# Optimization experiments

Measured on AMD Instinct MI355X. Metric: run time of the kernel, lower is better.

## Reference

```python
import jax, jax.numpy as jnp
import numpy as np

DN = ('NCHW', 'OIHW', 'NCHW')
LAP = jnp.array([[0., -1., 0.], [-1., 4., -1.], [0., -1., 0.]], dtype=jnp.float32).reshape(1, 1, 3, 3)
CH, NE = 24, 256


def conv(x, w, stride=1, pad=0):
    return jax.lax.conv_general_dilated(x, w, (stride, stride), ((pad, pad), (pad, pad)), dimension_numbers=DN)


def conv_t(x, w):
    # torch ConvTranspose2d(k=4, s=2, p=1); w is torch layout [in, out, 4, 4]
    wt = jnp.flip(w, (2, 3)).transpose(1, 0, 2, 3)
    return jax.lax.conv_general_dilated(x, wt, (1, 1), ((2, 2), (2, 2)), lhs_dilation=(2, 2), dimension_numbers=DN)


def spatial_attn(x, w_sa):
    y = jnp.concatenate([jnp.mean(x, 1, keepdims=True), jnp.max(x, 1, keepdims=True)], 1)
    return x * jax.nn.sigmoid(conv(y, w_sa, pad=3))


def res_branch(x, wr, wp, wsa):
    k = wr.shape[-1]
    h = conv(x, wr, pad=k // 2)
    h = conv(h, wp)
    return jax.nn.relu(spatial_attn(h, wsa))


def enc_block(x, wr, wp, wsa, wout):
    x = x + res_branch(x, wr, wp, wsa)
    return conv(x, wout, stride=2, pad=1)


def dec_block(x, wr, wp, wsa, wout):
    x = conv_t(x, wout)
    return x + res_branch(x, wr, wp, wsa)


def quantize(inp, embed):
    # inp: [B,H,W,D] tokens, embed: [D,N] codebook
    f = inp.reshape(-1, inp.shape[-1])
    dist = (f * f).sum(1, keepdims=True) - 2.0 * (f @ embed) + (embed * embed).sum(0, keepdims=True)
    ind = jnp.argmin(dist, axis=1)
    q = jnp.take(embed.T, ind, axis=0).reshape(inp.shape)
    diff = jnp.mean((jax.lax.stop_gradient(q) - inp) ** 2)
    q = inp + jax.lax.stop_gradient(q - inp)  # straight-through
    return q, diff


def _forward(x, w_img_in, w_img_out,
             w_res_et, w_pw_et, w_sa_et, w_out_et,
             w_res_em, w_pw_em, w_sa_em, w_out_em,
             w_res_ed, w_pw_ed, w_sa_ed, w_out_ed,
             w_res_dt, w_pw_dt, w_sa_dt, w_out_dt,
             w_res_dm, w_pw_dm, w_sa_dm, w_out_dm,
             w_res_dd, w_pw_dd, w_sa_dd, w_out_dd,
             w_squ1, w_squ2, embed2, embed3):
    xl = jax.lax.stop_gradient(conv(jnp.mean(x, 1, keepdims=True), LAP, pad=1))
    h = conv(xl, w_img_in)
    enc1 = enc_block(h, w_res_et, w_pw_et, w_sa_et, w_out_et)      # H/2
    enc2 = enc_block(enc1, w_res_em, w_pw_em, w_sa_em, w_out_em)   # H/4
    enc3 = enc_block(enc2, w_res_ed, w_pw_ed, w_sa_ed, w_out_ed)   # H/8
    qt2, d2 = quantize(enc2.transpose(0, 2, 3, 1), embed2)
    qt2 = qt2.transpose(0, 3, 1, 2)
    qt3, d3 = quantize(enc3.transpose(0, 2, 3, 1), embed3)
    qt3 = qt3.transpose(0, 3, 1, 2)
    dec3 = dec_block(qt3, w_res_dd, w_pw_dd, w_sa_dd, w_out_dd)    # H/4
    dec2 = conv(jnp.concatenate([dec3, qt2], 1), w_squ2)
    dec2 = dec_block(dec2, w_res_dm, w_pw_dm, w_sa_dm, w_out_dm)   # H/2
    dec1 = conv(jnp.concatenate([dec2, enc1], 1), w_squ1)
    dec1 = dec_block(dec1, w_res_dt, w_pw_dt, w_sa_dt, w_out_dt)   # H
    mask_lap = conv(dec1, w_img_out)
    clean_lap = xl - mask_lap
    return mask_lap, clean_lap, (d2 + d3).reshape(1)


def _param_shapes():
    shapes = {'w_img_in': (CH, 1, 1, 1), 'w_img_out': (1, CH, 1, 1),
              'w_squ1': (CH, 2 * CH, 1, 1), 'w_squ2': (CH, 2 * CH, 1, 1),
              'embed2': (CH, NE), 'embed3': (CH, NE)}
    for tag, k in [('et', 7), ('em', 5), ('ed', 3), ('dt', 7), ('dm', 5), ('dd', 3)]:
        shapes['w_res_' + tag] = (CH, CH, k, k)
        shapes['w_pw_' + tag] = (CH, CH, 1, 1)
        shapes['w_sa_' + tag] = (1, 2, 7, 7)
        shapes['w_out_' + tag] = (CH, CH, 4, 4)
    return shapes


def setup_inputs() -> dict:
    key = jax.random.key(0)
    shapes = _param_shapes()
    names = sorted(shapes)
    keys = jax.random.split(key, len(names) + 1)
    inputs = {'x': jax.random.normal(keys[0], (8, 3, 512, 512), dtype=jnp.float32)}
    for k_, name in zip(keys[1:], names):
        w = jax.random.normal(k_, shapes[name], dtype=jnp.float32)
        if not name.startswith('embed'):
            w = w * 0.05  # conv weight init scale
        inputs[name] = w
    return inputs


def reference(x, embed2, embed3, w_img_in, w_img_out,
              w_out_dd, w_out_dm, w_out_dt, w_out_ed, w_out_em, w_out_et,
              w_pw_dd, w_pw_dm, w_pw_dt, w_pw_ed, w_pw_em, w_pw_et,
              w_res_dd, w_res_dm, w_res_dt, w_res_ed, w_res_em, w_res_et,
              w_sa_dd, w_sa_dm, w_sa_dt, w_sa_ed, w_sa_em, w_sa_et,
              w_squ1, w_squ2):
    return _forward(x, w_img_in, w_img_out,
                    w_res_et, w_pw_et, w_sa_et, w_out_et,
                    w_res_em, w_pw_em, w_sa_em, w_out_em,
                    w_res_ed, w_pw_ed, w_sa_ed, w_out_ed,
                    w_res_dt, w_pw_dt, w_sa_dt, w_out_dt,
                    w_res_dm, w_pw_dm, w_sa_dm, w_out_dm,
                    w_res_dd, w_pw_dd, w_sa_dd, w_out_dd,
                    w_squ1, w_squ2, embed2, embed3)
```

## Files before the change

### kernel.cpp

```cpp
#include <hip/hip_runtime.h>
#include <math.h>

#define CH 24

typedef __attribute__((ext_vector_type(8))) short short8v;
typedef __attribute__((ext_vector_type(4))) float f32x4;
typedef unsigned short ushort_t;
typedef unsigned int uint_t;

__device__ inline ushort_t bf16r(float f){
  uint_t u = __float_as_uint(f);
  u += 0x7FFF + ((u>>16)&1);
  return (ushort_t)(u>>16);
}
__device__ inline float bf2f(uint_t u){ return __uint_as_float(u<<16); }

__global__ void k_r_res(const float* __restrict__ w, float* __restrict__ wT, int K){
  int i = blockIdx.x*256 + threadIdx.x;
  int n = 576*K*K; if (i >= n) return;
  int co = i % 24, ci = (i/24) % 24, kk = i/576;
  int ky = kk / K, kx = kk % K;
  wT[i] = w[((co*24+ci)*K+ky)*K+kx];
}
__global__ void k_r_pw(const float* __restrict__ w, float* __restrict__ wT, int CIN){
  int i = blockIdx.x*256 + threadIdx.x;
  if (i >= CIN*24) return;
  int co = i % 24, ci = i/24;
  wT[i] = w[co*CIN+ci];
}
__global__ void k_rmfma(const float* __restrict__ w, ushort_t* __restrict__ wb, int K){
  int i = blockIdx.x*256 + threadIdx.x;
  int n = K*K*1024; if (i >= n) return;
  int j = i & 7, l = (i>>3) & 63, t = (i>>9) & 1, tap = i >> 10;
  int ci = (l>>4)*8 + j, co = t*16 + (l&15);
  int ky = tap / K, kx = tap % K;
  float v = (ci<24 && co<24) ? w[((co*24+ci)*K+ky)*K+kx] : 0.f;
  wb[i] = bf16r(v);
}
__global__ void k_rmfma4(const float* __restrict__ w, ushort_t* __restrict__ wb){
  int i = blockIdx.x*256 + threadIdx.x;
  if (i >= 16384) return;
  int j = i & 7, l = (i>>3) & 63, t = (i>>9) & 1, tap = i >> 10;
  int ci = (l>>4)*8 + j, co = t*16 + (l&15);
  int ky = tap >> 2, kx = tap & 3;
  float v = (ci<24 && co<24) ? w[((ci*24+co)*4+ky)*4+kx] : 0.f;
  wb[i] = bf16r(v);
}


__global__ void k_lap(const float* __restrict__ x, float* __restrict__ xl, int H, int W){
  int idx = blockIdx.x*256 + threadIdx.x;
  int HW = H*W;
  if (idx >= HW) return;
  const float* xb = x + (size_t)blockIdx.z*3*HW;
  float* xo = xl + (size_t)blockIdx.z*HW;
  int px = idx % W, py = idx / W;
#define MEANV(yy,xx) (((yy)>=0&&(yy)<H&&(xx)>=0&&(xx)<W) ? (xb[(yy)*W+(xx)]+xb[HW+(yy)*W+(xx)]+xb[2*HW+(yy)*W+(xx)])*(1.f/3.f) : 0.f)
  float v = 4.f*MEANV(py,px) - MEANV(py-1,px) - MEANV(py+1,px) - MEANV(py,px-1) - MEANV(py,px+1);
#undef MEANV
  xo[idx] = v;
}

template<int K, bool EXPAND, bool INBF, bool OUTBF>
__launch_bounds__(512)
__global__ void k_conv_mfma(const void* in, const ushort_t* __restrict__ wb,
                            const ushort_t* __restrict__ wbpw, const float* __restrict__ wexp,
                            void* out, float* __restrict__ mm,
                            int H, int W, int istrIn, int istrOut, int istrMM){
  constexpr int SW_T = 32 + K - 1;
  constexpr int SH = 16 + K - 1;
  constexpr int NPX = SH*SW_T;
  __shared__ ushort_t lds[NPX*24];
  __shared__ uint_t sc[8][16*20];
  int tid = threadIdx.x;
  const float* inb_f = (const float*)in + (size_t)blockIdx.z*istrIn;
  const ushort_t* inb_b = (const ushort_t*)in + (size_t)blockIdx.z*istrIn;
  int x0g = blockIdx.x*32 - K/2, y0g = blockIdx.y*16 - K/2;
  int HW = H*W;
  for (int i = tid; i < NPX*3; i += 512){
    int q = i / NPX;
    int pp = i - q*NPX;
    int row = pp / SW_T, col = pp - row*SW_T;
    int gy = y0g + row, gx = x0g + col;
    uint4 w4; w4.x=0u; w4.y=0u; w4.z=0u; w4.w=0u;
    if (gy >= 0 && gy < H && gx >= 0 && gx < W){
      size_t base = (size_t)gy*W + gx;
      int c0 = q*8;
      if (EXPAND){
        float val = inb_f[base];
        w4.x = (uint_t)bf16r(val*wexp[c0+0]) | ((uint_t)bf16r(val*wexp[c0+1])<<16);
        w4.y = (uint_t)bf16r(val*wexp[c0+2]) | ((uint_t)bf16r(val*wexp[c0+3])<<16);
        w4.z = (uint_t)bf16r(val*wexp[c0+4]) | ((uint_t)bf16r(val*wexp[c0+5])<<16);
        w4.w = (uint_t)bf16r(val*wexp[c0+6]) | ((uint_t)bf16r(val*wexp[c0+7])<<16);
      } else if (INBF){
        uint_t u0=inb_b[(size_t)(c0+0)*HW+base], u1=inb_b[(size_t)(c0+1)*HW+base];
        uint_t u2=inb_b[(size_t)(c0+2)*HW+base], u3=inb_b[(size_t)(c0+3)*HW+base];
        uint_t u4=inb_b[(size_t)(c0+4)*HW+base], u5=inb_b[(size_t)(c0+5)*HW+base];
        uint_t u6=inb_b[(size_t)(c0+6)*HW+base], u7=inb_b[(size_t)(c0+7)*HW+base];
        w4.x = u0 | (u1<<16); w4.y = u2 | (u3<<16); w4.z = u4 | (u5<<16); w4.w = u6 | (u7<<16);
      } else {
        w4.x = (uint_t)bf16r(inb_f[(size_t)(c0+0)*HW+base]) | ((uint_t)bf16r(inb_f[(size_t)(c0+1)*HW+base])<<16);
        w4.y = (uint_t)bf16r(inb_f[(size_t)(c0+2)*HW+base]) | ((uint_t)bf16r(inb_f[(size_t)(c0+3)*HW+base])<<16);
        w4.z = (uint_t)bf16r(inb_f[(size_t)(c0+4)*HW+base]) | ((uint_t)bf16r(inb_f[(size_t)(c0+5)*HW+base])<<16);
        w4.w = (uint_t)bf16r(inb_f[(size_t)(c0+6)*HW+base]) | ((uint_t)bf16r(inb_f[(size_t)(c0+7)*HW+base])<<16);
      }
    }
// ... 192 lines not shown
}

template<bool INBF, bool OUTBF>
__launch_bounds__(512)
__global__ void k_down_mfma(const void* in, const ushort_t* __restrict__ wb,
                            void* out, int Ho, int Wo, int istrIn, int istrOut){
  const int Hi = Ho*2, Wi = Wo*2;
  constexpr int NPX = 18*34;
  __shared__ ushort_t lds[NPX*24];
  int tid = threadIdx.x;
  const float* inb_f = (const float*)in + (size_t)blockIdx.z*istrIn;
  const ushort_t* inb_b = (const ushort_t*)in + (size_t)blockIdx.z*istrIn;
  int X0 = blockIdx.x*16, Y0 = blockIdx.y*8;
  int ix0 = 2*X0 - 1, iy0 = 2*Y0 - 1;
  int HWi = Hi*Wi;
  for (int i = tid; i < NPX*3; i += 512){
    int q = i / NPX;
    int pp = i - q*NPX;
    int row = pp / 34;
    int rem = pp - row*34;
    int par = (rem >= 17) ? 1 : 0;
    int sub = rem - par*17;
    int gx = ix0 + 2*sub + par;
    int gy = iy0 + row;
    uint4 w4; w4.x=0u; w4.y=0u; w4.z=0u; w4.w=0u;
    if (gy>=0 && gy<Hi && gx>=0 && gx<Wi){
      size_t base = (size_t)gy*Wi + gx;
      int c0 = q*8;
      if (INBF){
        uint_t u0=inb_b[(size_t)(c0+0)*HWi+base], u1=inb_b[(size_t)(c0+1)*HWi+base];
        uint_t u2=inb_b[(size_t)(c0+2)*HWi+base], u3=inb_b[(size_t)(c0+3)*HWi+base];
        uint_t u4=inb_b[(size_t)(c0+4)*HWi+base], u5=inb_b[(size_t)(c0+5)*HWi+base];
        uint_t u6=inb_b[(size_t)(c0+6)*HWi+base], u7=inb_b[(size_t)(c0+7)*HWi+base];
        w4.x = u0 | (u1<<16); w4.y = u2 | (u3<<16); w4.z = u4 | (u5<<16); w4.w = u6 | (u7<<16);
      } else {
        w4.x = (uint_t)bf16r(inb_f[(size_t)(c0+0)*HWi+base]) | ((uint_t)bf16r(inb_f[(size_t)(c0+1)*HWi+base])<<16);
        w4.y = (uint_t)bf16r(inb_f[(size_t)(c0+2)*HWi+base]) | ((uint_t)bf16r(inb_f[(size_t)(c0+3)*HWi+base])<<16);
        w4.z = (uint_t)bf16r(inb_f[(size_t)(c0+4)*HWi+base]) | ((uint_t)bf16r(inb_f[(size_t)(c0+5)*HWi+base])<<16);
        w4.w = (uint_t)bf16r(inb_f[(size_t)(c0+6)*HWi+base]) | ((uint_t)bf16r(inb_f[(size_t)(c0+7)*HWi+base])<<16);
      }
    }
    *(uint4*)(lds + (size_t)pp*24 + q*8) = w4;
  }
  __syncthreads();
  int l = tid & 63, wid = tid >> 6;
  int kg = l >> 4, li = l & 15;
  int kgc = (kg < 3) ? kg : 2;
  f32x4 zero = {0.f,0.f,0.f,0.f};
  f32x4 acc0 = zero, acc1 = zero;
  const ushort_t* aln = lds + li*24 + kgc*8 + (size_t)(2*wid)*34*24;
  #pragma unroll
  for (int ky=0; ky<4; ky++){
    #pragma unroll
    for (int kx=0; kx<4; kx++){
      int tap = ky*4 + kx;
      const ushort_t* wp = wb + (size_t)tap*1024;
      short8v b0 = *(const short8v*)(wp + l*8);
      short8v b1 = *(const short8v*)(wp + 512 + l*8);
      short8v a = *(const short8v*)(aln + (ky*34 + (kx&1)*17 + (kx>>1))*24);
      acc0 = __builtin_amdgcn_mfma_f32_16x16x32_bf16(a, b0, acc0, 0, 0, 0);
      acc1 = __builtin_amdgcn_mfma_f32_16x16x32_bf16(a, b1, acc1, 0, 0, 0);
    }
  }
  int HWo = Ho*Wo;
  int oy = Y0 + wid, ox = X0 + kg*4;
  if (OUTBF){
    ushort_t* outb = (ushort_t*)out + (size_t)blockIdx.z*istrOut;
    uint2 p0; p0.x = (uint_t)bf16r(acc0[0]) | ((uint_t)bf16r(acc0[1])<<16);
    p0.y = (uint_t)bf16r(acc0[2]) | ((uint_t)bf16r(acc0[3])<<16);
    *(uint2*)(outb + (size_t)li*HWo + (size_t)oy*Wo + ox) = p0;
    if (li < 8){
      uint2 p1; p1.x = (uint_t)bf16r(acc1[0]) | ((uint_t)bf16r(acc1[1])<<16);
      p1.y = (uint_t)bf16r(acc1[2]) | ((uint_t)bf16r(acc1[3])<<16);
      *(uint2*)(outb + (size_t)(16+li)*HWo + (size_t)oy*Wo + ox) = p1;
    }
  } else {
    float* outb = (float*)out + (size_t)blockIdx.z*istrOut;
    *(f32x4*)(outb + (size_t)li*HWo + (size_t)oy*Wo + ox) = acc0;
    if (li < 8)
      *(f32x4*)(outb + (size_t)(16+li)*HWo + (size_t)oy*Wo + ox) = acc1;
  }
}

template<int K, int TH>
__launch_bounds__(256)
__global__ void k_conv(const float* __restrict__ in, const float* __restrict__ wT,
                       float* __restrict__ out, int H, int W, int istrIn, int istrOut){
  constexpr int TW = 32;
  constexpr int PX = (TW*TH)/256;
  constexpr int XT = TW/PX;
  constexpr int SW = TW + K - 1;
  constexpr int SWP = SW | 1;
  constexpr int SH = TH + K - 1;
  constexpr int CC = 8;
  __shared__ float tile[CC*SH*SWP];
  int tx = threadIdx.x % XT, ty = threadIdx.x / XT;
  int x0 = blockIdx.x*TW - K/2, y0 = blockIdx.y*TH - K/2;
  const float* inb = in + (size_t)blockIdx.z*istrIn;
  float acc[CH][PX];
  #pragma unroll
  for (int co=0;co<CH;co++)
    #pragma unroll
    for (int px=0;px<PX;px++) acc[co][px] = 0.f;

  #pragma unroll 1
  for (int c0=0;c0<CH;c0+=CC){
    __syncthreads();
    for (int i=threadIdx.x; i<CC*SH*SW; i+=256){
      int col = i % SW; int rr = i / SW; int row = rr % SH; int c = rr / SH;
      int gy = y0+row, gx = x0+col;
      tile[(c*SH+row)*SWP+col] = (gy>=0 && gy<H && gx>=0 && gx<W)
          ? inb[(size_t)(c0+c)*H*W + (size_t)gy*W + gx] : 0.f;
    }
    __syncthreads();
    #pragma unroll 1
    for (int ci=0;ci<CC;ci++){
      #pragma unroll 1
      for (int ky=0;ky<K;ky++){
        const float* trow = &tile[(ci*SH + ty+ky)*SWP + tx*PX];
        #pragma unroll
        for (int kx=0;kx<K;kx++){
          float v[PX];
          #pragma unroll
          for (int px=0;px<PX;px++) v[px] = trow[kx+px];
          const float* wp = wT + ((ky*K+kx)*24 + c0+ci)*24;
          #pragma unroll
          for (int co=0;co<CH;co++){
            float wv = wp[co];
            #pragma unroll
            for (int px=0;px<PX;px++) acc[co][px] = fmaf(v[px], wv, acc[co][px]);
          }
        }
      }
    }
  }
  int oy = blockIdx.y*TH+ty, ox = blockIdx.x*TW+tx*PX;
  float* ob = out + (size_t)blockIdx.z*istrOut + (size_t)oy*W + ox;
  #pragma unroll
  for (int co=0;co<CH;co++){
    if (PX == 2){
      float2 o; o.x=acc[co][0]; o.y=acc[co][1];
      *(float2*)(ob + (size_t)co*H*W) = o;
    } else {
      ob[(size_t)co*H*W] = acc[co][0];
    }
  }
}

__global__ void k_pw(const float* in, const float* __restrict__ wT,
                     float* out, float* __restrict__ mm, int HW, int istr, int istrMM){
  int p = (blockIdx.x*256 + threadIdx.x)*4;
  if (p >= HW) return;
  const float* ib = in + (size_t)blockIdx.z*istr;
  float acc[CH][4];
  #pragma unroll
  for (int co=0;co<CH;co++){ acc[co][0]=0;acc[co][1]=0;acc[co][2]=0;acc[co][3]=0; }
  #pragma unroll 1
  for (int ci=0;ci<CH;ci++){
    float4 v = *(const float4*)(ib + (size_t)ci*HW + p);
    const float* wp = wT + ci*24;
    #pragma unroll
    for (int co=0;co<CH;co++){
      float wv = wp[co];
      acc[co][0] = fmaf(v.x, wv, acc[co][0]);
      acc[co][1] = fmaf(v.y, wv, acc[co][1]);
      acc[co][2] = fmaf(v.z, wv, acc[co][2]);
      acc[co][3] = fmaf(v.w, wv, acc[co][3]);
    }
  }
  float mean[4]={0,0,0,0}, mx[4]={-3.4e38f,-3.4e38f,-3.4e38f,-3.4e38f};
  #pragma unroll
  for (int co=0;co<CH;co++)
    #pragma unroll
    for (int j=0;j<4;j++){ mean[j]+=acc[co][j]; mx[j]=fmaxf(mx[j],acc[co][j]); }
  float* ob = out + (size_t)blockIdx.z*istr;
  #pragma unroll
  for (int co=0;co<CH;co++){
    float4 o; o.x=acc[co][0]; o.y=acc[co][1]; o.z=acc[co][2]; o.w=acc[co][3];
    *(float4*)(ob + (size_t)co*HW + p) = o;
  }
  float* mb = mm + (size_t)blockIdx.z*istrMM;
  float4 me; me.x=mean[0]*(1.f/24.f); me.y=mean[1]*(1.f/24.f); me.z=mean[2]*(1.f/24.f); me.w=mean[3]*(1.f/24.f);
  float4 mxo; mxo.x=mx[0]; mxo.y=mx[1]; mxo.z=mx[2]; mxo.w=mx[3];
  *(float4*)(mb + p) = me;
  *(float4*)(mb + HW + p) = mxo;
}

template<bool BF>
__global__ void k_attn_res(const void* R_, const float* __restrict__ M,
                           const void* X_, const float* __restrict__ wsa,
                           void* out_, int H, int W, int istr, int istrMM){
  int p = (blockIdx.x*256 + threadIdx.x)*4;
  int HW = H*W;
  if (p >= HW) return;
  int py = p / W, px0 = p % W;
  const float* Mb = M + (size_t)blockIdx.z*istrMM;
  float s[4]={0,0,0,0};
  #pragma unroll
  for (int cc=0;cc<2;cc++){
    const float* Mc = Mb + (size_t)cc*HW;
    #pragma unroll 1
    for (int ky=0;ky<7;ky++){
      int gy = py+ky-3;
      if (gy<0||gy>=H) continue;
      const float* mr = Mc + (size_t)gy*W;
      float mv[10];
      #pragma unroll
      for (int j=0;j<10;j++){
        int gx = px0-3+j;
        mv[j] = (gx>=0 && gx<W) ? mr[gx] : 0.f;
      }
      const float* wr = wsa + (cc*7+ky)*7;
      #pragma unroll
      for (int kx=0;kx<7;kx++){
        float wv = wr[kx];
        #pragma unroll
        for (int px=0;px<4;px++) s[px] = fmaf(mv[kx+px], wv, s[px]);
      }
    }
  }
  float g[4];
  #pragma unroll
  for (int px=0;px<4;px++) g[px] = 1.f/(1.f+expf(-s[px]));
  #pragma unroll
  for (int c=0;c<CH;c++){
    float r0,r1,r2,r3, x0v,x1v,x2v,x3v;
    if (BF){
      const ushort_t* Rb = (const ushort_t*)R_ + (size_t)blockIdx.z*istr + (size_t)c*HW + p;
      const ushort_t* Xb = (const ushort_t*)X_ + (size_t)blockIdx.z*istr + (size_t)c*HW + p;
      uint2 rv = *(const uint2*)Rb;
      uint2 xv = *(const uint2*)Xb;
      r0=bf2f(rv.x&0xffffu); r1=bf2f(rv.x>>16); r2=bf2f(rv.y&0xffffu); r3=bf2f(rv.y>>16);
      x0v=bf2f(xv.x&0xffffu); x1v=bf2f(xv.x>>16); x2v=bf2f(xv.y&0xffffu); x3v=bf2f(xv.y>>16);
    } else {
      const float* Rb = (const float*)R_ + (size_t)blockIdx.z*istr + (size_t)c*HW + p;
      const float* Xb = (const float*)X_ + (size_t)blockIdx.z*istr + (size_t)c*HW + p;
      float4 rv = *(const float4*)Rb;
      float4 xv = *(const float4*)Xb;
      r0=rv.x; r1=rv.y; r2=rv.z; r3=rv.w;
      x0v=xv.x; x1v=xv.y; x2v=xv.z; x3v=xv.w;
    }
    float o0 = x0v + fmaxf(r0*g[0], 0.f);
    float o1 = x1v + fmaxf(r1*g[1], 0.f);
    float o2 = x2v + fmaxf(r2*g[2], 0.f);
    float o3 = x3v + fmaxf(r3*g[3], 0.f);
    if (BF){
      ushort_t* Ob = (ushort_t*)out_ + (size_t)blockIdx.z*istr + (size_t)c*HW + p;
      uint2 ov;
      ov.x = (uint_t)bf16r(o0) | ((uint_t)bf16r(o1)<<16);
      ov.y = (uint_t)bf16r(o2) | ((uint_t)bf16r(o3)<<16);
      *(uint2*)Ob = ov;
    } else {
      float* Ob = (float*)out_ + (size_t)blockIdx.z*istr + (size_t)c*HW + p;
      float4 ov; ov.x=o0; ov.y=o1; ov.z=o2; ov.w=o3;
      *(float4*)Ob = ov;
    }
  }
}

template<bool BF>
__global__ void k_attn_res_x(const void* R_, const float* __restrict__ M,
                             const float* __restrict__ XL, const float* __restrict__ wsa,
                             const float* __restrict__ wexp,
                             void* out_, int H, int W, int istr, int istrMM){
  int p = (blockIdx.x*256 + threadIdx.x)*4;
  int HW = H*W;
  if (p >= HW) return;
  int py = p / W, px0 = p % W;
  const float* Mb = M + (size_t)blockIdx.z*istrMM;
  float s[4]={0,0,0,0};
  #pragma unroll
  for (int cc=0;cc<2;cc++){
    const float* Mc = Mb + (size_t)cc*HW;
    #pragma unroll 1
    for (int ky=0;ky<7;ky++){
      int gy = py+ky-3;
      if (gy<0||gy>=H) continue;
      const float* mr = Mc + (size_t)gy*W;
      float mv[10];
      #pragma unroll
      for (int j=0;j<10;j++){
        int gx = px0-3+j;
        mv[j] = (gx>=0 && gx<W) ? mr[gx] : 0.f;
      }
      const float* wr = wsa + (cc*7+ky)*7;
      #pragma unroll
      for (int kx=0;kx<7;kx++){
        float wv = wr[kx];
        #pragma unroll
        for (int px=0;px<4;px++) s[px] = fmaf(mv[kx+px], wv, s[px]);
      }
    }
  }
  float g[4];
  #pragma unroll
  for (int px=0;px<4;px++) g[px] = 1.f/(1.f+expf(-s[px]));
  float4 xl4 = *(const float4*)(XL + (size_t)blockIdx.z*HW + p);
  #pragma unroll
  for (int c=0;c<CH;c++){
    float wc = wexp[c];
    float r0,r1,r2,r3;
    if (BF){
      const ushort_t* Rb = (const ushort_t*)R_ + (size_t)blockIdx.z*istr + (size_t)c*HW + p;
      uint2 rv = *(const uint2*)Rb;
      r0=bf2f(rv.x&0xffffu); r1=bf2f(rv.x>>16); r2=bf2f(rv.y&0xffffu); r3=bf2f(rv.y>>16);
    } else {
      const float* Rb = (const float*)R_ + (size_t)blockIdx.z*istr + (size_t)c*HW + p;
      float4 rv = *(const float4*)Rb;
      r0=rv.x; r1=rv.y; r2=rv.z; r3=rv.w;
    }
    float o0 = xl4.x*wc + fmaxf(r0*g[0], 0.f);
    float o1 = xl4.y*wc + fmaxf(r1*g[1], 0.f);
    float o2 = xl4.z*wc + fmaxf(r2*g[2], 0.f);
    float o3 = xl4.w*wc + fmaxf(r3*g[3], 0.f);
    if (BF){
      ushort_t* Ob = (ushort_t*)out_ + (size_t)blockIdx.z*istr + (size_t)c*HW + p;
      uint2 ov;
      ov.x = (uint_t)bf16r(o0) | ((uint_t)bf16r(o1)<<16);
      ov.y = (uint_t)bf16r(o2) | ((uint_t)bf16r(o3)<<16);
      *(uint2*)Ob = ov;
    } else {
      float* Ob = (float*)out_ + (size_t)blockIdx.z*istr + (size_t)c*HW + p;
      float4 ov; ov.x=o0; ov.y=o1; ov.z=o2; ov.w=o3;
      *(float4*)Ob = ov;
    }
  }
}

template<bool BF>
__global__ void k_squeeze(const void* inA_, const void* inB_,
                          const float* __restrict__ wT, void* out_, int HW, int istr){
  int p = (blockIdx.x*256 + threadIdx.x)*4;
  if (p >= HW) return;
  float acc[CH][4];
  #pragma unroll
  for (int co=0;co<CH;co++){ acc[co][0]=0;acc[co][1]=0;acc[co][2]=0;acc[co][3]=0; }
  #pragma unroll 1
  for (int ci=0;ci<48;ci++){
    float v0,v1,v2,v3;
    if (BF){
      const ushort_t* src = (ci<24)
        ? ((const ushort_t*)inA_ + (size_t)blockIdx.z*istr + (size_t)ci*HW + p)
        : ((const ushort_t*)inB_ + (size_t)blockIdx.z*istr + (size_t)(ci-24)*HW + p);
      uint2 rv = *(const uint2*)src;
      v0=bf2f(rv.x&0xffffu); v1=bf2f(rv.x>>16); v2=bf2f(rv.y&0xffffu); v3=bf2f(rv.y>>16);
    } else {
      const float* src = (ci<24)
        ? ((const float*)inA_ + (size_t)blockIdx.z*istr + (size_t)ci*HW + p)
        : ((const float*)inB_ + (size_t)blockIdx.z*istr + (size_t)(ci-24)*HW + p);
      float4 rv = *(const float4*)src;
      v0=rv.x; v1=rv.y; v2=rv.z; v3=rv.w;
    }
    const float* wp = wT + ci*24;
    #pragma unroll
    for (int co=0;co<CH;co++){
      float wv = wp[co];
      acc[co][0] = fmaf(v0, wv, acc[co][0]);
      acc[co][1] = fmaf(v1, wv, acc[co][1]);
      acc[co][2] = fmaf(v2, wv, acc[co][2]);
      acc[co][3] = fmaf(v3, wv, acc[co][3]);
    }
  }
  #pragma unroll
  for (int co=0;co<CH;co++){
    if (BF){
      ushort_t* ob = (ushort_t*)out_ + (size_t)blockIdx.z*istr + (size_t)co*HW + p;
      uint2 ov;
      ov.x = (uint_t)bf16r(acc[co][0]) | ((uint_t)bf16r(acc[co][1])<<16);
      ov.y = (uint_t)bf16r(acc[co][2]) | ((uint_t)bf16r(acc[co][3])<<16);
      *(uint2*)ob = ov;
    } else {
      float* ob = (float*)out_ + (size_t)blockIdx.z*istr + (size_t)co*HW + p;
      float4 o; o.x=acc[co][0]; o.y=acc[co][1]; o.z=acc[co][2]; o.w=acc[co][3];
      *(float4*)ob = o;
    }
  }
}

__global__ void k_quant(const float* __restrict__ enc, const float* __restrict__ embed,
                        float* __restrict__ qt, float* __restrict__ diffAcc, int HW, int istr){
  __shared__ float em[256*28];
  __shared__ float red[4];
  {
    int j = threadIdx.x;
    float s = 0.f;
    #pragma unroll
    for (int c=0;c<CH;c++){
      float e = embed[c*256+j];
      em[j*28+c] = -2.0f*e;
      s = fmaf(e,e,s);
    }
    em[j*28+24] = s; em[j*28+25]=0.f; em[j*28+26]=0.f; em[j*28+27]=0.f;
  }
  __syncthreads();
  int p = blockIdx.x*256 + threadIdx.x;
  const float* eb = enc + (size_t)blockIdx.z*istr;
  float f[CH];
  #pragma unroll
  for (int c=0;c<CH;c++) f[c] = eb[(size_t)c*HW + p];
  float best = 3.4e38f; int bj = 0;
  #pragma unroll 1
  for (int j=0;j<256;j++){
    const float4* row = (const float4*)&em[j*28];
    float s = em[j*28+24];
    #pragma unroll
    for (int q4=0;q4<6;q4++){
      float4 r = row[q4];
      s = fmaf(f[q4*4+0], r.x, s);
      s = fmaf(f[q4*4+1], r.y, s);
      s = fmaf(f[q4*4+2], r.z, s);
      s = fmaf(f[q4*4+3], r.w, s);
    }
    if (s < best){ best = s; bj = j; }
  }
  float* qb = qt + (size_t)blockIdx.z*istr;
  float d = 0.f;
  #pragma unroll
  for (int c=0;c<CH;c++){
    float q = embed[c*256+bj];
    qb[(size_t)c*HW + p] = q;
    float e = q - f[c];
    d = fmaf(e,e,d);
  }
  #pragma unroll
  for (int off=32; off>0; off>>=1) d += __shfl_down(d, off, 64);
  int lane = threadIdx.x & 63, wv = threadIdx.x >> 6;
  if (lane==0) red[wv] = d;
  __syncthreads();
  if (threadIdx.x==0) atomicAdd(diffAcc, red[0]+red[1]+red[2]+red[3]);
}

__global__ void k_final(const ushort_t* __restrict__ dec1, const float* __restrict__ w,
                        const float* __restrict__ xl, float* __restrict__ outMask,
                        float* __restrict__ outClean, int HW, int dstr){
  int p = (blockIdx.x*256 + threadIdx.x)*4;
  if (p >= HW) return;
  const ushort_t* db = dec1 + (size_t)blockIdx.z*dstr;
  float m[4]={0,0,0,0};
  #pragma unroll
  for (int c=0;c<CH;c++){
    uint2 dv = *(const uint2*)(db + (size_t)c*HW + p);
    float wc = w[c];
    m[0]=fmaf(bf2f(dv.x&0xffffu),wc,m[0]);
    m[1]=fmaf(bf2f(dv.x>>16),wc,m[1]);
    m[2]=fmaf(bf2f(dv.y&0xffffu),wc,m[2]);
    m[3]=fmaf(bf2f(dv.y>>16),wc,m[3]);
  }
  float4 xv = *(const float4*)(xl + (size_t)blockIdx.z*HW + p);
  float4 mo; mo.x=m[0]; mo.y=m[1]; mo.z=m[2]; mo.w=m[3];
  float4 co; co.x=xv.x-m[0]; co.y=xv.y-m[1]; co.z=xv.z-m[2]; co.w=xv.w-m[3];
  *(float4*)(outMask + (size_t)blockIdx.z*HW + p) = mo;
  *(float4*)(outClean + (size_t)blockIdx.z*HW + p) = co;
}

__global__ void k_diff(const float* __restrict__ acc, float* __restrict__ out){
  out[0] = acc[0]*(1.f/3145728.f) + acc[1]*(1.f/786432.f);
}

extern "C" void kernel_launch(void* const* d_in, const int* in_sizes, int n_in,
                              void* d_out, int out_size, void* d_ws, size_t ws_size,
                              hipStream_t stream) {
  const float* x        = (const float*)d_in[0];
  const float* embed2   = (const float*)d_in[1];
  const float* embed3   = (const float*)d_in[2];
  const float* w_img_in = (const float*)d_in[3];
  const float* w_img_out= (const float*)d_in[4];
  const float* w_out_dd = (const float*)d_in[5];
  const float* w_out_dm = (const float*)d_in[6];
  const float* w_out_dt = (const float*)d_in[7];
  const float* w_out_ed = (const float*)d_in[8];
  const float* w_out_em = (const float*)d_in[9];
  const float* w_out_et = (const float*)d_in[10];
  const float* w_pw_dd  = (const float*)d_in[11];
  const float* w_pw_dm  = (const float*)d_in[12];
  const float* w_pw_dt  = (const float*)d_in[13];
  const float* w_pw_ed  = (const float*)d_in[14];
  const float* w_pw_em  = (const float*)d_in[15];
  const float* w_pw_et  = (const float*)d_in[16];
  const float* w_res_dd = (const float*)d_in[17];
  const float* w_res_dm = (const float*)d_in[18];
  const float* w_res_dt = (const float*)d_in[19];
  const float* w_res_ed = (const float*)d_in[20];
  const float* w_res_em = (const float*)d_in[21];
  const float* w_res_et = (const float*)d_in[22];
  const float* w_sa_dd  = (const float*)d_in[23];
  const float* w_sa_dm  = (const float*)d_in[24];
  const float* w_sa_dt  = (const float*)d_in[25];
  const float* w_sa_ed  = (const float*)d_in[26];
  const float* w_sa_em  = (const float*)d_in[27];
  const float* w_sa_et  = (const float*)d_in[28];
  const float* w_squ1   = (const float*)d_in[29];
  const float* w_squ2   = (const float*)d_in[30];
  (void)in_sizes; (void)n_in; (void)out_size;

  const int HW512 = 512*512, HW256 = 256*256, HW128 = 128*128, HW64 = 64*64;
  const int S512 = 24*HW512, S256 = 24*HW256, S128 = 24*HW128, S64 = 24*HW64;

  float* ws = (float*)d_ws;
  float* OUT = (float*)d_out;
  size_t F = ws_size / sizeof(float);

  float* WT      = ws;
  float* wt_ed3  = WT + 85248;
  float* wt_dd3  = WT + 90432;
  float* wt_pw_ed= WT + 152064;
  float* wt_pw_dd= WT + 152640;
  float* wt_squ1 = WT + 154368;
  float* wt_squ2 = WT + 155520;

  ushort_t* WB = (ushort_t*)(ws + 160000);
  ushort_t* wb_et7   = WB;
  ushort_t* wb_dt7   = WB + 50176;
  ushort_t* wb_em5   = WB + 100352;
  ushort_t* wb_dm5   = WB + 125952;
  ushort_t* wb_pw_et = WB + 151552;
  ushort_t* wb_pw_em = WB + 152576;
  ushort_t* wb_pw_dm = WB + 153600;
  ushort_t* wb_pw_dt = WB + 154624;
  ushort_t* wb4_dd   = WB + 155648;
  ushort_t* wb4_dm   = WB + 172032;
  ushort_t* wb4_dt   = WB + 188416;
  ushort_t* wb4d_et  = WB + 204800;
  ushort_t* wb4d_em  = WB + 221184;
  ushort_t* wb4d_ed  = WB + 237568;

  const size_t ABASE = 290000;

  auto needBatched = [&](size_t CB)->size_t{
    size_t u_f = (CB*(size_t)S512 + 1)/2;
    if ((size_t)4*S256 > u_f) u_f = (size_t)4*S256;
    if ((size_t)8*S128 > u_f) u_f = (size_t)8*S128;
    return ABASE + 2097152 + (size_t)4*S256 + 3145728 + 786432 + CB*524288 + 2*u_f + 2;
  };
  int CB = 0;
  if (F >= needBatched(8)) CB = 8;
  else if (F >= needBatched(4)) CB = 4;
  else if (F >= needBatched(2)) CB = 2;
  const size_t NEED_B = ABASE + 15925250;
  if (CB == 0 && F < NEED_B) return;

  float *XL, *E2, *Q2, *E3, *Q3, *MM, *DIFF, *U1, *U2;
  ushort_t* E1b;
  if (CB > 0){
    size_t off = ABASE;
    size_t u_f = (CB*(size_t)S512 + 1)/2;
    if ((size_t)4*S256 > u_f) u_f = (size_t)4*S256;
    if ((size_t)8*S128 > u_f) u_f = (size_t)8*S128;
    XL = ws + off; off += 2097152;
    E1b = (ushort_t*)(ws + off); off += (size_t)4*S256;
    Q2 = ws + off; off += 3145728;
    Q3 = ws + off; off += 786432;
    MM = ws + off; off += CB*524288;
    U1 = ws + off; off += u_f;
    U2 = ws + off; off += u_f;
    DIFF = ws + off;
    E2 = OUT;
    E3 = OUT + 3145728;
  } else {
    size_t off = ABASE;
    XL = ws + off; off += 262144;
    U1 = ws + off; off += 6291456;
    U2 = ws + off; off += 6291456;
    E1b = (ushort_t*)(ws + off); off += 1572864;
    E2 = ws + off; off += 393216;
    Q2 = ws + off; off += 393216;
    E3 = ws + off; off += 98304;
    Q3 = ws + off; off += 98304;
    MM = ws + off; off += 524288;
    DIFF = ws + off;
  }
  ushort_t* U1b = (ushort_t*)U1;
  ushort_t* U2b = (ushort_t*)U2;

  k_rmfma<<<dim3(196), 256, 0, stream>>>(w_res_et, wb_et7, 7);
  k_rmfma<<<dim3(196), 256, 0, stream>>>(w_res_dt, wb_dt7, 7);
  k_rmfma<<<dim3(100), 256, 0, stream>>>(w_res_em, wb_em5, 5);
  k_rmfma<<<dim3(100), 256, 0, stream>>>(w_res_dm, wb_dm5, 5);
  k_rmfma<<<dim3(4), 256, 0, stream>>>(w_pw_et, wb_pw_et, 1);
  k_rmfma<<<dim3(4), 256, 0, stream>>>(w_pw_em, wb_pw_em, 1);
  k_rmfma<<<dim3(4), 256, 0, stream>>>(w_pw_dm, wb_pw_dm, 1);
  k_rmfma<<<dim3(4), 256, 0, stream>>>(w_pw_dt, wb_pw_dt, 1);
  k_rmfma4<<<dim3(64), 256, 0, stream>>>(w_out_dd, wb4_dd);
  k_rmfma4<<<dim3(64), 256, 0, stream>>>(w_out_dm, wb4_dm);
  k_rmfma4<<<dim3(64), 256, 0, stream>>>(w_out_dt, wb4_dt);
  k_rmfma<<<dim3(64), 256, 0, stream>>>(w_out_et, wb4d_et, 4);
  k_rmfma<<<dim3(64), 256, 0, stream>>>(w_out_em, wb4d_em, 4);
  k_rmfma<<<dim3(64), 256, 0, stream>>>(w_out_ed, wb4d_ed, 4);
  k_r_res<<<dim3((576*9+255)/256), 256, 0, stream>>>(w_res_ed, wt_ed3, 3);
  k_r_res<<<dim3((576*9+255)/256), 256, 0, stream>>>(w_res_dd, wt_dd3, 3);
  k_r_pw<<<dim3(3), 256, 0, stream>>>(w_pw_ed, wt_pw_ed, 24);
  k_r_pw<<<dim3(3), 256, 0, stream>>>(w_pw_dd, wt_pw_dd, 24);
  k_r_pw<<<dim3(5), 256, 0, stream>>>(w_squ1, wt_squ1, 48);
  k_r_pw<<<dim3(5), 256, 0, stream>>>(w_squ2, wt_squ2, 48);

  hipMemsetAsync(DIFF, 0, 2*sizeof(float), stream);

  auto phase1 = [&](int c0, int nz, float* XLp, ushort_t* E1p){
    k_lap<<<dim3(HW512/256,1,nz), 256, 0, stream>>>(x + (size_t)c0*3*HW512, XLp, 512, 512);
    k_conv_mfma<7,true,false,true><<<dim3(16,32,nz), 512, 0, stream>>>(
        XLp, wb_et7, wb_pw_et, w_img_in, U2b, MM, 512, 512, HW512, S512, 2*HW512);
    k_attn_res_x<true><<<dim3(HW512/1024,1,nz), 256, 0, stream>>>(
        U2b, MM, XLp, w_sa_et, w_img_in, U1b, 512, 512, S512, 2*HW512);
    k_down_mfma<true,true><<<dim3(16,32,nz), 512, 0, stream>>>(U1b, wb4d_et, E1p, 256, 256, S512, S256);
  };

  auto deep = [&](int nb, ushort_t* E1p, float* SAp, float* SBp, float* E2p, float* Q2p,
                  float* E3p, float* Q3p, float* MMp, ushort_t* D1p){
    ushort_t* SAb = (ushort_t*)SAp;
    ushort_t* SBb = (ushort_t*)SBp;
    int mm256 = 2*HW256, mm128 = 2*HW128;
    k_conv_mfma<5,false,true,true><<<dim3(8,16,nb), 512, 0, stream>>>(
        E1p, wb_em5, wb_pw_em, nullptr, SAb, MMp, 256, 256, S256, S256, mm256);
    k_attn_res<true><<<dim3(HW256/1024,1,nb), 256, 0, stream>>>(SAb, MMp, E1p, w_sa_em, SBb, 256, 256, S256, mm256);
    k_down_mfma<true,false><<<dim3(8,16,nb), 512, 0, stream>>>(SBb, wb4d_em, E2p, 128, 128, S256, S128);
    k_conv<3,8><<<dim3(4,16,nb), 256, 0, stream>>>(E2p, wt_ed3, SAp, 128, 128, S128, S128);
    k_pw<<<dim3(HW128/1024,1,nb), 256, 0, stream>>>(SAp, wt_pw_ed, SAp, MMp, HW128, S128, mm128);
    k_attn_res<false><<<dim3(HW128/1024,1,nb), 256, 0, stream>>>(SAp, MMp, E2p, w_sa_ed, SBp, 128, 128, S128, mm128);
    k_down_mfma<false,false><<<dim3(4,8,nb), 512, 0, stream>>>(SBp, wb4d_ed, E3p, 64, 64, S128, S64);
    k_quant<<<dim3(HW128/256,1,nb), 256, 0, stream>>>(E2p, embed2, Q2p, DIFF+0, HW128, S128);
    k_quant<<<dim3(HW64/256,1,nb), 256, 0, stream>>>(E3p, embed3, Q3p, DIFF+1, HW64, S64);
    k_convT_mfma<false,false><<<dim3(4,8,nb), 512, 0, stream>>>(Q3p, wb4_dd, SAp, 128, 128, S64, S128);
    k_conv<3,8><<<dim3(4,16,nb), 256, 0, stream>>>(SAp, wt_dd3, SBp, 128, 128, S128, S128);
    k_pw<<<dim3(HW128/1024,1,nb), 256, 0, stream>>>(SBp, wt_pw_dd, SBp, MMp, HW128, S128, mm128);
    k_attn_res<false><<<dim3(HW128/1024,1,nb), 256, 0, stream>>>(SBp, MMp, SAp, w_sa_dd, SAp, 128, 128, S128, mm128);
    k_squeeze<false><<<dim3(HW128/1024,1,nb), 256, 0, stream>>>(SAp, Q2p, wt_squ2, SBp, HW128, S128);
    k_convT_mfma<false,true><<<dim3(8,16,nb), 512, 0, stream>>>(SBp, wb4_dm, SAb, 256, 256, S128, S256);
    k_conv_mfma<5,false,true,true><<<dim3(8,16,nb), 512, 0, stream>>>(
        SAb, wb_dm5, wb_pw_dm, nullptr, SBb, MMp, 256, 256, S256, S256, mm256);
    k_attn_res<true><<<dim3(HW256/1024,1,nb), 256, 0, stream>>>(SBb, MMp, SAb, w_sa_dm, SAb, 256, 256, S256, mm256);
    k_squeeze<true><<<dim3(HW256/1024,1,nb), 256, 0, stream>>>(SAb, E1p, wt_squ1, D1p, HW256, S256);
  };

  auto phase3 = [&](int c0, int nz, const ushort_t* D1p, const float* XLp){
    k_convT_mfma<true,true><<<dim3(16,32,nz), 512, 0, stream>>>(D1p, wb4_dt, U1b, 512, 512, S256, S512);
    k_conv_mfma<7,false,true,true><<<dim3(16,32,nz), 512, 0, stream>>>(
        U1b, wb_dt7, wb_pw_dt, nullptr, U2b, MM, 512, 512, S512, S512, 2*HW512);
    k_attn_res<true><<<dim3(HW512/1024,1,nz), 256, 0, stream>>>(U2b, MM, U1b, w_sa_dt, U1b, 512, 512, S512, 2*HW512);
    k_final<<<dim3(HW512/1024,1,nz), 256, 0, stream>>>(U1b, w_img_out, XLp,
                                                       OUT + (size_t)c0*HW512,
                                                       OUT + 2097152 + (size_t)c0*HW512,
                                                       HW512, S512);
  };

  if (CB > 0){
    for (int c0=0;c0<8;c0+=CB)
      phase1(c0, CB, XL + (size_t)c0*HW512, E1b + (size_t)c0*S256);
    deep(8, E1b, U1, U2, E2, Q2, E3, Q3, MM, E1b);
    for (int c0=0;c0<8;c0+=CB)
      phase3(c0, CB, E1b + (size_t)c0*S256, XL + (size_t)c0*HW512);
  } else {
    for (int b=0;b<8;b++){
      phase1(b, 1, XL, E1b);
      deep(1, E1b, U1, U2, E2, Q2, E3, Q3, MM, (ushort_t*)U2);
      phase3(b, 1, (ushort_t*)U2, XL);
    }
  }

  k_diff<<<1, 1, 0, stream>>>(DIFF, OUT + 4194304);
}
```

Before: 1.440 ms.

## Move 128x128 res convs to MFMA and fuse final attention with output projection

Replaces the scalar fp32 3x3 conv plus separate pointwise kernel at 128x128 resolution with the existing fused MFMA conv+pointwise kernel, using bf16-packed weights. It also fuses the last spatial-attention residual with the final 1x1 output projection, so the 512x512 bf16 activation is no longer written and then reread. The cost is bf16 rounding of weights and inputs in the 128x128 convs, which shifts numerics slightly.

```diff
diff --git a/kernel.cpp b/kernel.cpp
--- a/kernel.cpp
+++ b/kernel.cpp
@@ -15,13 +15,6 @@
 }
 __device__ inline float bf2f(uint_t u){ return __uint_as_float(u<<16); }
 
-__global__ void k_r_res(const float* __restrict__ w, float* __restrict__ wT, int K){
-  int i = blockIdx.x*256 + threadIdx.x;
-  int n = 576*K*K; if (i >= n) return;
-  int co = i % 24, ci = (i/24) % 24, kk = i/576;
-  int ky = kk / K, kx = kk % K;
-  wT[i] = w[((co*24+ci)*K+ky)*K+kx];
-}
 __global__ void k_r_pw(const float* __restrict__ w, float* __restrict__ wT, int CIN){
   int i = blockIdx.x*256 + threadIdx.x;
   if (i >= CIN*24) return;
@@ -380,110 +373,6 @@
   }
 }
 
-template<int K, int TH>
-__launch_bounds__(256)
-__global__ void k_conv(const float* __restrict__ in, const float* __restrict__ wT,
-                       float* __restrict__ out, int H, int W, int istrIn, int istrOut){
-  constexpr int TW = 32;
-  constexpr int PX = (TW*TH)/256;
-  constexpr int XT = TW/PX;
-  constexpr int SW = TW + K - 1;
-  constexpr int SWP = SW | 1;
-  constexpr int SH = TH + K - 1;
-  constexpr int CC = 8;
-  __shared__ float tile[CC*SH*SWP];
-  int tx = threadIdx.x % XT, ty = threadIdx.x / XT;
-  int x0 = blockIdx.x*TW - K/2, y0 = blockIdx.y*TH - K/2;
-  const float* inb = in + (size_t)blockIdx.z*istrIn;
-  float acc[CH][PX];
-  #pragma unroll
-  for (int co=0;co<CH;co++)
-    #pragma unroll
-    for (int px=0;px<PX;px++) acc[co][px] = 0.f;
-
-  #pragma unroll 1
-  for (int c0=0;c0<CH;c0+=CC){
-    __syncthreads();
-    for (int i=threadIdx.x; i<CC*SH*SW; i+=256){
-      int col = i % SW; int rr = i / SW; int row = rr % SH; int c = rr / SH;
-      int gy = y0+row, gx = x0+col;
-      tile[(c*SH+row)*SWP+col] = (gy>=0 && gy<H && gx>=0 && gx<W)
-          ? inb[(size_t)(c0+c)*H*W + (size_t)gy*W + gx] : 0.f;
-    }
-    __syncthreads();
-    #pragma unroll 1
-    for (int ci=0;ci<CC;ci++){
-      #pragma unroll 1
-      for (int ky=0;ky<K;ky++){
-        const float* trow = &tile[(ci*SH + ty+ky)*SWP + tx*PX];
-        #pragma unroll
-        for (int kx=0;kx<K;kx++){
-          float v[PX];
-          #pragma unroll
-          for (int px=0;px<PX;px++) v[px] = trow[kx+px];
-          const float* wp = wT + ((ky*K+kx)*24 + c0+ci)*24;
-          #pragma unroll
-          for (int co=0;co<CH;co++){
-            float wv = wp[co];
-            #pragma unroll
-            for (int px=0;px<PX;px++) acc[co][px] = fmaf(v[px], wv, acc[co][px]);
-          }
-        }
-      }
-    }
-  }
-  int oy = blockIdx.y*TH+ty, ox = blockIdx.x*TW+tx*PX;
-  float* ob = out + (size_t)blockIdx.z*istrOut + (size_t)oy*W + ox;
-  #pragma unroll
-  for (int co=0;co<CH;co++){
-    if (PX == 2){
-      float2 o; o.x=acc[co][0]; o.y=acc[co][1];
-      *(float2*)(ob + (size_t)co*H*W) = o;
-    } else {
-      ob[(size_t)co*H*W] = acc[co][0];
-    }
-  }
-}
-
-__global__ void k_pw(const float* in, const float* __restrict__ wT,
-                     float* out, float* __restrict__ mm, int HW, int istr, int istrMM){
-  int p = (blockIdx.x*256 + threadIdx.x)*4;
-  if (p >= HW) return;
-  const float* ib = in + (size_t)blockIdx.z*istr;
-  float acc[CH][4];
-  #pragma unroll
-  for (int co=0;co<CH;co++){ acc[co][0]=0;acc[co][1]=0;acc[co][2]=0;acc[co][3]=0; }
-  #pragma unroll 1
-  for (int ci=0;ci<CH;ci++){
-    float4 v = *(const float4*)(ib + (size_t)ci*HW + p);
-    const float* wp = wT + ci*24;
-    #pragma unroll
-    for (int co=0;co<CH;co++){
-      float wv = wp[co];
-      acc[co][0] = fmaf(v.x, wv, acc[co][0]);
-      acc[co][1] = fmaf(v.y, wv, acc[co][1]);
-      acc[co][2] = fmaf(v.z, wv, acc[co][2]);
-      acc[co][3] = fmaf(v.w, wv, acc[co][3]);
-    }
-  }
-  float mean[4]={0,0,0,0}, mx[4]={-3.4e38f,-3.4e38f,-3.4e38f,-3.4e38f};
-  #pragma unroll
-  for (int co=0;co<CH;co++)
-    #pragma unroll
-    for (int j=0;j<4;j++){ mean[j]+=acc[co][j]; mx[j]=fmaxf(mx[j],acc[co][j]); }
-  float* ob = out + (size_t)blockIdx.z*istr;
-  #pragma unroll
-  for (int co=0;co<CH;co++){
-    float4 o; o.x=acc[co][0]; o.y=acc[co][1]; o.z=acc[co][2]; o.w=acc[co][3];
-    *(float4*)(ob + (size_t)co*HW + p) = o;
-  }
-  float* mb = mm + (size_t)blockIdx.z*istrMM;
-  float4 me; me.x=mean[0]*(1.f/24.f); me.y=mean[1]*(1.f/24.f); me.z=mean[2]*(1.f/24.f); me.w=mean[3]*(1.f/24.f);
-  float4 mxo; mxo.x=mx[0]; mxo.y=mx[1]; mxo.z=mx[2]; mxo.w=mx[3];
-  *(float4*)(mb + p) = me;
-  *(float4*)(mb + HW + p) = mxo;
-}
-
 template<bool BF>
 __global__ void k_attn_res(const void* R_, const float* __restrict__ M,
                            const void* X_, const float* __restrict__ wsa,
@@ -625,6 +514,64 @@
   }
 }
 
+__global__ void k_attn_final(const ushort_t* __restrict__ R, const float* __restrict__ M,
+                             const ushort_t* __restrict__ X, const float* __restrict__ wsa,
+                             const float* __restrict__ wout, const float* __restrict__ xl,
+                             float* __restrict__ outMask, float* __restrict__ outClean,
+                             int H, int W, int istr, int istrMM){
+  int p = (blockIdx.x*256 + threadIdx.x)*4;
+  int HW = H*W;
+  if (p >= HW) return;
+  int py = p / W, px0 = p % W;
+  const float* Mb = M + (size_t)blockIdx.z*istrMM;
+  float s[4]={0,0,0,0};
+  #pragma unroll
+  for (int cc=0;cc<2;cc++){
+    const float* Mc = Mb + (size_t)cc*HW;
+    #pragma unroll 1
+    for (int ky=0;ky<7;ky++){
+      int gy = py+ky-3;
+      if (gy<0||gy>=H) continue;
+      const float* mr = Mc + (size_t)gy*W;
+      float mv[10];
+      #pragma unroll
+      for (int j=0;j<10;j++){
+        int gx = px0-3+j;
+        mv[j] = (gx>=0 && gx<W) ? mr[gx] : 0.f;
+      }
+      const float* wr = wsa + (cc*7+ky)*7;
+      #pragma unroll
+      for (int kx=0;kx<7;kx++){
+        float wv = wr[kx];
+        #pragma unroll
+        for (int px=0;px<4;px++) s[px] = fmaf(mv[kx+px], wv, s[px]);
+      }
+    }
+  }
+  float g[4];
+  #pragma unroll
+  for (int px=0;px<4;px++) g[px] = 1.f/(1.f+expf(-s[px]));
+  float m0=0.f,m1=0.f,m2=0.f,m3=0.f;
+  #pragma unroll
+  for (int c=0;c<CH;c++){
+    const ushort_t* Rb = R + (size_t)blockIdx.z*istr + (size_t)c*HW + p;
+    const ushort_t* Xb = X + (size_t)blockIdx.z*istr + (size_t)c*HW + p;
+    uint2 rv = *(const uint2*)Rb;
+    uint2 xv = *(const uint2*)Xb;
+    float wc = wout[c];
+    float o0 = bf2f(xv.x&0xffffu) + fmaxf(bf2f(rv.x&0xffffu)*g[0], 0.f);
+    float o1 = bf2f(xv.x>>16)     + fmaxf(bf2f(rv.x>>16)*g[1], 0.f);
+    float o2 = bf2f(xv.y&0xffffu) + fmaxf(bf2f(rv.y&0xffffu)*g[2], 0.f);
+    float o3 = bf2f(xv.y>>16)     + fmaxf(bf2f(rv.y>>16)*g[3], 0.f);
+    m0 = fmaf(o0,wc,m0); m1 = fmaf(o1,wc,m1); m2 = fmaf(o2,wc,m2); m3 = fmaf(o3,wc,m3);
+  }
+  float4 xlv = *(const float4*)(xl + (size_t)blockIdx.z*HW + p);
+  float4 mo; mo.x=m0; mo.y=m1; mo.z=m2; mo.w=m3;
+  float4 co; co.x=xlv.x-m0; co.y=xlv.y-m1; co.z=xlv.z-m2; co.w=xlv.w-m3;
+  *(float4*)(outMask + (size_t)blockIdx.z*HW + p) = mo;
+  *(float4*)(outClean + (size_t)blockIdx.z*HW + p) = co;
+}
+
 template<bool BF>
 __global__ void k_squeeze(const void* inA_, const void* inB_,
                           const float* __restrict__ wT, void* out_, int HW, int istr){
@@ -726,29 +673,6 @@
   if (lane==0) red[wv] = d;
   __syncthreads();
   if (threadIdx.x==0) atomicAdd(diffAcc, red[0]+red[1]+red[2]+red[3]);
-}
-
-__global__ void k_final(const ushort_t* __restrict__ dec1, const float* __restrict__ w,
-                        const float* __restrict__ xl, float* __restrict__ outMask,
-                        float* __restrict__ outClean, int HW, int dstr){
-  int p = (blockIdx.x*256 + threadIdx.x)*4;
-  if (p >= HW) return;
-  const ushort_t* db = dec1 + (size_t)blockIdx.z*dstr;
-  float m[4]={0,0,0,0};
-  #pragma unroll
-  for (int c=0;c<CH;c++){
-    uint2 dv = *(const uint2*)(db + (size_t)c*HW + p);
-    float wc = w[c];
-    m[0]=fmaf(bf2f(dv.x&0xffffu),wc,m[0]);
-    m[1]=fmaf(bf2f(dv.x>>16),wc,m[1]);
-    m[2]=fmaf(bf2f(dv.y&0xffffu),wc,m[2]);
-    m[3]=fmaf(bf2f(dv.y>>16),wc,m[3]);
-  }
-  float4 xv = *(const float4*)(xl + (size_t)blockIdx.z*HW + p);
-  float4 mo; mo.x=m[0]; mo.y=m[1]; mo.z=m[2]; mo.w=m[3];
-  float4 co; co.x=xv.x-m[0]; co.y=xv.y-m[1]; co.z=xv.z-m[2]; co.w=xv.w-m[3];
-  *(float4*)(outMask + (size_t)blockIdx.z*HW + p) = mo;
-  *(float4*)(outClean + (size_t)blockIdx.z*HW + p) = co;
 }
 
 __global__ void k_diff(const float* __restrict__ acc, float* __restrict__ out){
@@ -799,10 +723,6 @@
   size_t F = ws_size / sizeof(float);
 
   float* WT      = ws;
-  float* wt_ed3  = WT + 85248;
-  float* wt_dd3  = WT + 90432;
-  float* wt_pw_ed= WT + 152064;
-  float* wt_pw_dd= WT + 152640;
   float* wt_squ1 = WT + 154368;
   float* wt_squ2 = WT + 155520;
 
@@ -821,8 +741,12 @@
   ushort_t* wb4d_et  = WB + 204800;
   ushort_t* wb4d_em  = WB + 221184;
   ushort_t* wb4d_ed  = WB + 237568;
-
-  const size_t ABASE = 290000;
+  ushort_t* wb_ed3   = WB + 253952;
+  ushort_t* wb_dd3   = WB + 263168;
+  ushort_t* wb_pw_ed = WB + 272384;
+  ushort_t* wb_pw_dd = WB + 273408;
+
+  const size_t ABASE = 300000;
 
   auto needBatched = [&](size_t CB)->size_t{
     size_t u_f = (CB*(size_t)S512 + 1)/2;
@@ -874,20 +798,20 @@
   k_rmfma<<<dim3(196), 256, 0, stream>>>(w_res_dt, wb_dt7, 7);
   k_rmfma<<<dim3(100), 256, 0, stream>>>(w_res_em, wb_em5, 5);
   k_rmfma<<<dim3(100), 256, 0, stream>>>(w_res_dm, wb_dm5, 5);
+  k_rmfma<<<dim3(36), 256, 0, stream>>>(w_res_ed, wb_ed3, 3);
+  k_rmfma<<<dim3(36), 256, 0, stream>>>(w_res_dd, wb_dd3, 3);
   k_rmfma<<<dim3(4), 256, 0, stream>>>(w_pw_et, wb_pw_et, 1);
   k_rmfma<<<dim3(4), 256, 0, stream>>>(w_pw_em, wb_pw_em, 1);
   k_rmfma<<<dim3(4), 256, 0, stream>>>(w_pw_dm, wb_pw_dm, 1);
   k_rmfma<<<dim3(4), 256, 0, stream>>>(w_pw_dt, wb_pw_dt, 1);
+  k_rmfma<<<dim3(4), 256, 0, stream>>>(w_pw_ed, wb_pw_ed, 1);
+  k_rmfma<<<dim3(4), 256, 0, stream>>>(w_pw_dd, wb_pw_dd, 1);
   k_rmfma4<<<dim3(64), 256, 0, stream>>>(w_out_dd, wb4_dd);
   k_rmfma4<<<dim3(64), 256, 0, stream>>>(w_out_dm, wb4_dm);
   k_rmfma4<<<dim3(64), 256, 0, stream>>>(w_out_dt, wb4_dt);
   k_rmfma<<<dim3(64), 256, 0, stream>>>(w_out_et, wb4d_et, 4);
   k_rmfma<<<dim3(64), 256, 0, stream>>>(w_out_em, wb4d_em, 4);
   k_rmfma<<<dim3(64), 256, 0, stream>>>(w_out_ed, wb4d_ed, 4);
-  k_r_res<<<dim3((576*9+255)/256), 256, 0, stream>>>(w_res_ed, wt_ed3, 3);
-  k_r_res<<<dim3((576*9+255)/256), 256, 0, stream>>>(w_res_dd, wt_dd3, 3);
-  k_r_pw<<<dim3(3), 256, 0, stream>>>(w_pw_ed, wt_pw_ed, 24);
-  k_r_pw<<<dim3(3), 256, 0, stream>>>(w_pw_dd, wt_pw_dd, 24);
   k_r_pw<<<dim3(5), 256, 0, stream>>>(w_squ1, wt_squ1, 48);
   k_r_pw<<<dim3(5), 256, 0, stream>>>(w_squ2, wt_squ2, 48);
 
@@ -911,15 +835,15 @@
         E1p, wb_em5, wb_pw_em, nullptr, SAb, MMp, 256, 256, S256, S256, mm256);
     k_attn_res<true><<<dim3(HW256/1024,1,nb), 256, 0, stream>>>(SAb, MMp, E1p, w_sa_em, SBb, 256, 256, S256, mm256);
     k_down_mfma<true,false><<<dim3(8,16,nb), 512, 0, stream>>>(SBb, wb4d_em, E2p, 128, 128, S256, S128);
-    k_conv<3,8><<<dim3(4,16,nb), 256, 0, stream>>>(E2p, wt_ed3, SAp, 128, 128, S128, S128);
-    k_pw<<<dim3(HW128/1024,1,nb), 256, 0, stream>>>(SAp, wt_pw_ed, SAp, MMp, HW128, S128, mm128);
+    k_conv_mfma<3,false,false,false><<<dim3(4,8,nb), 512, 0, stream>>>(
+        E2p, wb_ed3, wb_pw_ed, nullptr, SAp, MMp, 128, 128, S128, S128, mm128);
     k_attn_res<false><<<dim3(HW128/1024,1,nb), 256, 0, stream>>>(SAp, MMp, E2p, w_sa_ed, SBp, 128, 128, S128, mm128);
     k_down_mfma<false,false><<<dim3(4,8,nb), 512, 0, stream>>>(SBp, wb4d_ed, E3p, 64, 64, S128, S64);
     k_quant<<<dim3(HW128/256,1,nb), 256, 0, stream>>>(E2p, embed2, Q2p, DIFF+0, HW128, S128);
     k_quant<<<dim3(HW64/256,1,nb), 256, 0, stream>>>(E3p, embed3, Q3p, DIFF+1, HW64, S64);
     k_convT_mfma<false,false><<<dim3(4,8,nb), 512, 0, stream>>>(Q3p, wb4_dd, SAp, 128, 128, S64, S128);
-    k_conv<3,8><<<dim3(4,16,nb), 256, 0, stream>>>(SAp, wt_dd3, SBp, 128, 128, S128, S128);
-    k_pw<<<dim3(HW128/1024,1,nb), 256, 0, stream>>>(SBp, wt_pw_dd, SBp, MMp, HW128, S128, mm128);
+    k_conv_mfma<3,false,false,false><<<dim3(4,8,nb), 512, 0, stream>>>(
+        SAp, wb_dd3, wb_pw_dd, nullptr, SBp, MMp, 128, 128, S128, S128, mm128);
     k_attn_res<false><<<dim3(HW128/1024,1,nb), 256, 0, stream>>>(SBp, MMp, SAp, w_sa_dd, SAp, 128, 128, S128, mm128);
     k_squeeze<false><<<dim3(HW128/1024,1,nb), 256, 0, stream>>>(SAp, Q2p, wt_squ2, SBp, HW128, S128);
     k_convT_mfma<false,true><<<dim3(8,16,nb), 512, 0, stream>>>(SBp, wb4_dm, SAb, 256, 256, S128, S256);
@@ -933,11 +857,10 @@
     k_convT_mfma<true,true><<<dim3(16,32,nz), 512, 0, stream>>>(D1p, wb4_dt, U1b, 512, 512, S256, S512);
     k_conv_mfma<7,false,true,true><<<dim3(16,32,nz), 512, 0, stream>>>(
         U1b, wb_dt7, wb_pw_dt, nullptr, U2b, MM, 512, 512, S512, S512, 2*HW512);
-    k_attn_res<true><<<dim3(HW512/1024,1,nz), 256, 0, stream>>>(U2b, MM, U1b, w_sa_dt, U1b, 512, 512, S512, 2*HW512);
-    k_final<<<dim3(HW512/1024,1,nz), 256, 0, stream>>>(U1b, w_img_out, XLp,
-                                                       OUT + (size_t)c0*HW512,
-                                                       OUT + 2097152 + (size_t)c0*HW512,
-                                                       HW512, S512);
+    k_attn_final<<<dim3(HW512/1024,1,nz), 256, 0, stream>>>(
+        U2b, MM, U1b, w_sa_dt, w_img_out, XLp,
+        OUT + (size_t)c0*HW512, OUT + 2097152 + (size_t)c0*HW512,
+        512, 512, S512, 2*HW512);
   };
 
   if (CB > 0){
```

Measured after the change: 1.311 ms. 9.0% less time.
